# Performance work log

Measured on AMD Instinct MI355X. Metric: run time of the kernel, lower is better.

Reference implementation:

```python
import jax, jax.numpy as jnp
import numpy as np
from jax import lax

T_D = 0.7          # condensation radius
T_B = 0.2          # min beta to seed a condensate
FEATURE_LENGTH = 9 # columns of raw features before the prediction block
N_FEAT = 17        # n_ccoords = N_FEAT - 14 = 3
N_EVENTS = 16
POINTS_PER_EVENT = 65536


def setup_inputs() -> dict:
    key = jax.random.key(0)
    N = N_EVENTS * POINTS_PER_EVENT
    # uniform [0,1): betas in [0,1), ccoords in the unit cube -> realistic clustering
    x = jax.random.uniform(key, (N, N_FEAT), dtype=jnp.float32)
    row_splits = (jnp.arange(N_EVENTS + 1) * POINTS_PER_EVENT).astype(jnp.int32)
    return {"x": x, "row_splits": row_splits}


def _build_condensates(ccoords, betas, radius, min_beta):
    """Greedy NMS-like condensation, vectorized over events.
    ccoords: [E, P, C] float; betas: [E, P] float.
    Returns asso [E,P] int32 (index of assigned condensate, -1 = noise) and
    iscond [E,P] bool (condensation point flags).
    """
    E, P, _ = ccoords.shape
    r2 = radius * radius

    def masked_beta(asso):
        return jnp.where(asso < 0, betas, -1.0)

    def cond_fn(state):
        asso, _ = state
        return jnp.any(jnp.max(masked_beta(asso), axis=1) >= min_beta)

    def body_fn(state):
        asso, iscond = state
        mb = masked_beta(asso)                     # [E,P]
        ref = jnp.argmax(mb, axis=1)               # [E] highest-beta unassigned point
        valid = jnp.take_along_axis(mb, ref[:, None], axis=1)[:, 0] >= min_beta  # [E]
        refc = jnp.take_along_axis(ccoords, ref[:, None, None], axis=1)          # [E,1,C]
        distsq = jnp.sum((ccoords - refc) ** 2, axis=-1)                          # [E,P]
        assign = (asso < 0) & (distsq <= r2) & valid[:, None]
        asso = jnp.where(assign, ref[:, None].astype(jnp.int32), asso)
        newcond = (jnp.arange(P)[None, :] == ref[:, None]) & valid[:, None]
        return asso, iscond | newcond

    asso0 = jnp.full((E, P), -1, dtype=jnp.int32)
    iscond0 = jnp.zeros((E, P), dtype=jnp.bool_)
    return lax.while_loop(cond_fn, body_fn, (asso0, iscond0))


def reference(x, row_splits):
    E = row_splits.shape[0] - 1
    N, F = x.shape
    P = N // E  # uniform events (RaggedConstructTensor equivalent for equal splits)
    n_ccoords = F - 14
    x_pred = x[:, FEATURE_LENGTH:]
    n_pred = x_pred.shape[-1]
    betas = x_pred[:, 0].reshape(E, P)
    ccoords = x_pred[:, n_pred - n_ccoords:].reshape(E, P, n_ccoords)

    asso, iscond = _build_condensates(ccoords, betas, T_D, T_B)

    ncond = jnp.sum(iscond, axis=1).astype(jnp.int32)  # condensates per event
    out_row_splits = jnp.concatenate(
        [jnp.zeros((1,), jnp.int32), jnp.cumsum(ncond).astype(jnp.int32)])
    # jit-safe equivalent of dout = x[iscond > 0]: zero-mask non-condensates
    mask = iscond.reshape(-1, 1).astype(x.dtype)
    dout = x * mask  # [N, F], rows of non-condensates are zero
    return dout, out_row_splits
```

## Files before the change

### kernel.cpp

```cpp
#include <hip/hip_runtime.h>

typedef unsigned long long u64;
typedef unsigned int u32;

static constexpr int NF = 17;
static constexpr int BCOL = 9;
static constexpr int CCOL = 14;
static constexpr int CONDCAP = 256;
static constexpr int NPASS = 4;
static constexpr int RPB = 512;
static constexpr int MAXIT = 8;

#define T_B_F ((float)0.2)
#define R2_F  ((float)(0.7*0.7))

__device__ __forceinline__ u64 kmax(u64 a, u64 b){ return a > b ? a : b; }

__device__ __forceinline__ u64 shfl_down_u64(u64 v, int off){
    u32 lo = (u32)v, hi = (u32)(v >> 32);
    lo = __shfl_down(lo, off, 64);
    hi = __shfl_down(hi, off, 64);
    return ((u64)hi << 32) | lo;
}

__device__ __forceinline__ u64 waveReduceMax(u64 k){
    #pragma unroll
    for (int off = 32; off > 0; off >>= 1){
        u64 o = shfl_down_u64(k, off);
        if (o > k) k = o;
    }
    return k;
}

__device__ __forceinline__ float dist2(float cx, float cy, float cz,
                                       float rx, float ry, float rz){
    #pragma clang fp contract(off)
    float dx = cx - rx, dy = cy - ry, dz = cz - rz;
    float sx = dx * dx, sy = dy * dy, sz = dz * dz;
    return (sx + sy) + sz;
}

__device__ __forceinline__ u64 makeKey(float beta, u32 idx){
    return ((u64)__float_as_uint(beta) << 32) | (u64)(0xFFFFFFFFu - idx);
}

__global__ void k_init(u32* ws){
    int t = threadIdx.x;
    if (t < 1024) ws[t] = 0;
}

__global__ __launch_bounds__(512) void k_filter(
    const float4* __restrict__ x4, float4* __restrict__ out4,
    u64* __restrict__ argmax0, int* __restrict__ cnt0,
    float4* __restrict__ cA, int* __restrict__ iA,
    int P, int chunksPerEvent)
{
    __shared__ float lds[RPB * NF];
    __shared__ int swc[8], swb[8], sbase;
    __shared__ u64 sred[8];

    int e = blockIdx.x / chunksPerEvent;
    int chunk = blockIdx.x % chunksPerEvent;
    int rowStart = chunk * RPB;
    size_t tile4 = (size_t)blockIdx.x * (RPB * NF / 4);

    float4* lds4 = (float4*)lds;
    const int N4 = RPB * NF / 4;
    float4 z = make_float4(0.f, 0.f, 0.f, 0.f);
    for (int i = threadIdx.x; i < N4; i += 512){
        lds4[i] = x4[tile4 + i];
        out4[tile4 + i] = z;
    }
    __syncthreads();

    int tid = threadIdx.x, lid = tid & 63, wid = tid >> 6;
    float be = lds[tid*NF+BCOL];
    float cx = lds[tid*NF+CCOL], cy = lds[tid*NF+CCOL+1], cz = lds[tid*NF+CCOL+2];
    bool kp = (be >= T_B_F);
    u64 bal = __ballot(kp);
    int wcnt = __popcll(bal);
    u64 lk = kp ? makeKey(be, (u32)(rowStart + tid)) : 0;
    u64 kw = waveReduceMax(lk);
    if (lid == 0){ swc[wid] = wcnt; sred[wid] = kw; }
    __syncthreads();
    if (tid == 0){
        int tot = 0;
        for (int w = 0; w < 8; w++){ swb[w] = tot; tot += swc[w]; }
        sbase = tot ? atomicAdd(&cnt0[e], tot) : 0;
        u64 m = sred[0];
        for (int i = 1; i < 8; i++) m = kmax(m, sred[i]);
        if (m) atomicMax(&argmax0[e], m);
    }
    __syncthreads();
    if (kp){
        int pos = sbase + swb[wid] + __popcll(bal & ((1ull << lid) - 1));
        size_t eoff = (size_t)e * P;
        cA[eoff + pos] = make_float4(cx, cy, cz, be);
        iA[eoff + pos] = rowStart + tid;
    }
}

__global__ __launch_bounds__(256) void k_pass(
    const float* __restrict__ x,
    const float4* __restrict__ cIn, const int* __restrict__ iIn,
    float4* __restrict__ cOut, int* __restrict__ iOut,
    const u64* __restrict__ argmaxIn, u64* __restrict__ argmaxOut,
    const int* __restrict__ cntIn, int* __restrict__ cntOut,
    int* __restrict__ ncond, int* __restrict__ condlist,
    int P, int blocksPerEvent)
{
    __shared__ int swc[4], swb[4], sbase;
    __shared__ u64 sred[4];

    int e = blockIdx.x / blocksPerEvent;
    int c = blockIdx.x % blocksPerEvent;
    u64 key = argmaxIn[e];
    float betaRef = __uint_as_float((u32)(key >> 32));
    if (!(betaRef >= T_B_F)) return;
    u32 refIdx = 0xFFFFFFFFu - (u32)(key & 0xFFFFFFFFu);
    if (c == 0 && threadIdx.x == 0){
        int s = atomicAdd(&ncond[e], 1);
        if (s < CONDCAP) condlist[e * CONDCAP + s] = (int)refIdx;
    }
    int n = cntIn[e];
    if (c * 256 >= n) return;
    size_t rbase = ((size_t)e * P + refIdx) * NF;
    float rx = x[rbase + CCOL], ry = x[rbase + CCOL + 1], rz = x[rbase + CCOL + 2];

    int tid = threadIdx.x, lid = tid & 63, wid = tid >> 6;
    size_t eoff = (size_t)e * P;
    int stride = blocksPerEvent * 256;

    float4 cc[MAXIT]; int ix[MAXIT]; bool kp[MAXIT]; u64 bal[MAXIT];
    int wcnt = 0;
    u64 lk = 0;
    #pragma unroll
    for (int k = 0; k < MAXIT; k++){
        int i = c * 256 + tid + k * stride;
        bool inb = i < n;
        int ii = inb ? i : 0;
        cc[k] = cIn[eoff + ii];
        ix[k] = iIn[eoff + ii];
        float d2 = dist2(cc[k].x, cc[k].y, cc[k].z, rx, ry, rz);
        kp[k] = inb && !(d2 <= R2_F);
        bal[k] = __ballot(kp[k]);
        wcnt += __popcll(bal[k]);
        if (kp[k]) lk = kmax(lk, makeKey(cc[k].w, (u32)ix[k]));
    }
    u64 kw = waveReduceMax(lk);
    if (lid == 0){ swc[wid] = wcnt; sred[wid] = kw; }
    __syncthreads();
    if (tid == 0){
        int tot = 0;
        for (int w = 0; w < 4; w++){ swb[w] = tot; tot += swc[w]; }
        sbase = tot ? atomicAdd(&cntOut[e], tot) : 0;
        u64 m = sred[0];
        for (int i = 1; i < 4; i++) m = kmax(m, sred[i]);
        if (m) atomicMax(&argmaxOut[e], m);
    }
    __syncthreads();
    int pos = sbase + swb[wid];
    u64 lm = (1ull << lid) - 1;
    #pragma unroll
    for (int k = 0; k < MAXIT; k++){
        if (kp[k]){
            int p_ = pos + __popcll(bal[k] & lm);
            cOut[eoff + p_] = cc[k];
            iOut[eoff + p_] = ix[k];
        }
        pos += __popcll(bal[k]);
    }
}

__global__ __launch_bounds__(1024) void k_finish(
    const float* __restrict__ x,
    float4* cA, int* iA, float4* cB, int* iB,
    const u64* __restrict__ argmax2, const int* __restrict__ cnt2,
    int* __restrict__ ncond, int* __restrict__ condlist, int P)
{
    int e = blockIdx.x;
    __shared__ u64 sred[16];
    __shared__ int scnt;
    __shared__ u64 skey;
    __shared__ float srefc[3];

    int n = cnt2[e];
    u64 key = argmax2[e];
    float4* cIn = cA + (size_t)e * P; int* iIn = iA + (size_t)e * P;
    float4* cOut = cB + (size_t)e * P; int* iOut = iB + (size_t)e * P;
    int tid = threadIdx.x, lid = tid & 63, wid = tid >> 6;

    while (true){
        float betaRef = __uint_as_float((u32)(key >> 32));
        if (!(betaRef >= T_B_F)) break;
        u32 refIdx = 0xFFFFFFFFu - (u32)(key & 0xFFFFFFFFu);
        if (tid == 0){
            int s = atomicAdd(&ncond[e], 1);
            if (s < CONDCAP) condlist[e * CONDCAP + s] = (int)refIdx;
            size_t rbase = ((size_t)e * P + refIdx) * NF;
            srefc[0] = x[rbase + CCOL];
            srefc[1] = x[rbase + CCOL + 1];
            srefc[2] = x[rbase + CCOL + 2];
            scnt = 0;
        }
        __syncthreads();
        float rx = srefc[0], ry = srefc[1], rz = srefc[2];
        u64 localKey = 0;
        for (int i = tid; i < n; i += 1024){
            float4 cc = cIn[i]; int idx = iIn[i];
            float d2 = dist2(cc.x, cc.y, cc.z, rx, ry, rz);
            bool keep = !(d2 <= R2_F);
            u64 bal = __ballot(keep);
            int cw = __popcll(bal);
            int b_ = 0;
            if (lid == 0) b_ = cw ? atomicAdd(&scnt, cw) : 0;
            b_ = __shfl(b_, 0, 64);
            if (keep){
                int pos = b_ + __popcll(bal & ((1ull << lid) - 1));
                cOut[pos] = cc; iOut[pos] = idx;
                localKey = kmax(localKey, makeKey(cc.w, (u32)idx));
            }
        }
        u64 kw = waveReduceMax(localKey);
        if (lid == 0) sred[wid] = kw;
        __syncthreads();
        if (tid == 0){
            u64 m = 0;
            for (int i = 0; i < 16; i++) m = kmax(m, sred[i]);
            skey = m;
        }
        __syncthreads();
        key = skey;
        n = scnt;
        { float4* t = cIn; cIn = cOut; cOut = t; }
        { int* t = iIn; iIn = iOut; iOut = t; }
        __syncthreads();
    }
}

__global__ void k_out(const float* __restrict__ x, float* __restrict__ out,
                      const int* __restrict__ ncond, const int* __restrict__ condlist,
                      int P, int E)
{
    int e = blockIdx.x;
    if (e == 0 && threadIdx.x < E + 1){
        int s = 0;
        for (int i = 0; i < (int)threadIdx.x; i++) s += ncond[i];
        out[(size_t)E * P * NF + threadIdx.x] = (float)s;
    }
    int nc = ncond[e];
    if (nc > CONDCAP) nc = CONDCAP;
    int tot = nc * NF;
    for (int i = threadIdx.x; i < tot; i += blockDim.x){
        int j = i / NF, f = i - j * NF;
        int row = condlist[e * CONDCAP + j];
        size_t base = ((size_t)e * P + row) * NF;
        out[base + f] = x[base + f];
    }
}

extern "C" void kernel_launch(void* const* d_in, const int* in_sizes, int n_in,
                              void* d_out, int out_size, void* d_ws, size_t ws_size,
                              hipStream_t stream) {
    const float* x = (const float*)d_in[0];
    int N = in_sizes[0] / NF;
    int E = in_sizes[1] - 1;
    int P = N / E;
    float* out = (float*)d_out;
    char* ws = (char*)d_ws;

    u64* argmax = (u64*)ws;
    int* cnt    = (int*)(ws + 1024);
    int* ncond  = (int*)(ws + 2048);
    int* condlist = (int*)(ws + 4096);
    size_t listOff = 32768;
    size_t listElems = (size_t)E * P;
    float4* cA = (float4*)(ws + listOff);
    float4* cB = (float4*)(ws + listOff + listElems * 16);
    int* iA = (int*)(ws + listOff + listElems * 32);
    int* iB = (int*)(ws + listOff + listElems * 36);

    k_init<<<1, 1024, 0, stream>>>((u32*)ws);

    int chunksPerEvent = P / RPB;
    k_filter<<<E * chunksPerEvent, 512, 0, stream>>>(
        (const float4*)x, (float4*)out, argmax, cnt, cA, iA, P, chunksPerEvent);

    int bpe = 32;
    float4* cs[2] = {cA, cB};
    int* is[2] = {iA, iB};
    for (int r = 0; r < NPASS; r++){
        k_pass<<<E * bpe, 256, 0, stream>>>(
            x, cs[r & 1], is[r & 1], cs[(r + 1) & 1], is[(r + 1) & 1],
            argmax + r * E, argmax + (r + 1) * E,
            cnt + r * E, cnt + (r + 1) * E,
            ncond, condlist, P, bpe);
    }

    k_finish<<<E, 1024, 0, stream>>>(
        x, cA, iA, cB, iB, argmax + NPASS * E, cnt + NPASS * E, ncond, condlist, P);

    k_out<<<E, 256, 0, stream>>>(x, out, ncond, condlist, P, E);
}
```

Before: 188.2 us.

## Run greedy condensation tail in LDS, batch four refs per round, fuse output

Measured after the change: 246.4 us. 30.9% more time.

```diff
diff --git a/kernel.cpp b/kernel.cpp
--- a/kernel.cpp
+++ b/kernel.cpp
@@ -2,6 +2,7 @@
 
 typedef unsigned long long u64;
 typedef unsigned int u32;
+typedef float nfloat4 __attribute__((ext_vector_type(4)));
 
 static constexpr int NF = 17;
 static constexpr int BCOL = 9;
@@ -10,6 +11,9 @@
 static constexpr int NPASS = 4;
 static constexpr int RPB = 512;
 static constexpr int MAXIT = 8;
+static constexpr int LCAP = 7168;
+static constexpr int FT = 1024;
+static constexpr int FSLOT = 7;
 
 #define T_B_F ((float)0.2)
 #define R2_F  ((float)(0.7*0.7))
@@ -20,6 +24,13 @@
     u32 lo = (u32)v, hi = (u32)(v >> 32);
     lo = __shfl_down(lo, off, 64);
     hi = __shfl_down(hi, off, 64);
+    return ((u64)hi << 32) | lo;
+}
+
+__device__ __forceinline__ u64 shfl_u64(u64 v, int lane){
+    u32 lo = (u32)v, hi = (u32)(v >> 32);
+    lo = __shfl(lo, lane, 64);
+    hi = __shfl(hi, lane, 64);
     return ((u64)hi << 32) | lo;
 }
 
@@ -66,10 +77,10 @@
 
     float4* lds4 = (float4*)lds;
     const int N4 = RPB * NF / 4;
-    float4 z = make_float4(0.f, 0.f, 0.f, 0.f);
+    nfloat4 z = (nfloat4)0.f;
     for (int i = threadIdx.x; i < N4; i += 512){
         lds4[i] = x4[tile4 + i];
-        out4[tile4 + i] = z;
+        __builtin_nontemporal_store(z, (nfloat4*)&out4[tile4 + i]);
     }
     __syncthreads();
 
@@ -175,28 +186,39 @@
 __global__ __launch_bounds__(1024) void k_finish(
     const float* __restrict__ x,
     float4* cA, int* iA, float4* cB, int* iB,
-    const u64* __restrict__ argmax2, const int* __restrict__ cnt2,
-    int* __restrict__ ncond, int* __restrict__ condlist, int P)
+    const u64* __restrict__ argmaxN, const int* __restrict__ cntN,
+    int* __restrict__ ncond, const int* __restrict__ condlistG,
+    int* __restrict__ done, float* __restrict__ out, int P, int E)
 {
+    __shared__ u64 skey[LCAP];
+    __shared__ float sx[LCAP], sy[LCAP], sz[LCAP];
+    __shared__ u64 sred[16];
+    __shared__ u64 wtopk[16*4];
+    __shared__ int wtopp[16*4];
+    __shared__ int condL[CONDCAP];
+    __shared__ float refs[4][3];
+    __shared__ int scnt, snc, snacc;
+    __shared__ u64 skeyb;
+    __shared__ float srefc[3];
+
     int e = blockIdx.x;
-    __shared__ u64 sred[16];
-    __shared__ int scnt;
-    __shared__ u64 skey;
-    __shared__ float srefc[3];
-
-    int n = cnt2[e];
-    u64 key = argmax2[e];
+    int tid = threadIdx.x, lid = tid & 63, wid = tid >> 6;
+    int n = cntN[e];
+    u64 key = argmaxN[e];
     float4* cIn = cA + (size_t)e * P; int* iIn = iA + (size_t)e * P;
     float4* cOut = cB + (size_t)e * P; int* iOut = iB + (size_t)e * P;
-    int tid = threadIdx.x, lid = tid & 63, wid = tid >> 6;
-
-    while (true){
+
+    if (tid == 0) snc = ncond[e];
+    for (int i = tid; i < CONDCAP; i += FT) condL[i] = condlistG[e * CONDCAP + i];
+    __syncthreads();
+
+    while (n > LCAP){
         float betaRef = __uint_as_float((u32)(key >> 32));
         if (!(betaRef >= T_B_F)) break;
         u32 refIdx = 0xFFFFFFFFu - (u32)(key & 0xFFFFFFFFu);
         if (tid == 0){
-            int s = atomicAdd(&ncond[e], 1);
-            if (s < CONDCAP) condlist[e * CONDCAP + s] = (int)refIdx;
+            if (snc < CONDCAP) condL[snc] = (int)refIdx;
+            snc++;
             size_t rbase = ((size_t)e * P + refIdx) * NF;
             srefc[0] = x[rbase + CCOL];
             srefc[1] = x[rbase + CCOL + 1];
@@ -206,7 +228,7 @@
         __syncthreads();
         float rx = srefc[0], ry = srefc[1], rz = srefc[2];
         u64 localKey = 0;
-        for (int i = tid; i < n; i += 1024){
+        for (int i = tid; i < n; i += FT){
             float4 cc = cIn[i]; int idx = iIn[i];
             float d2 = dist2(cc.x, cc.y, cc.z, rx, ry, rz);
             bool keep = !(d2 <= R2_F);
@@ -227,35 +249,139 @@
         if (tid == 0){
             u64 m = 0;
             for (int i = 0; i < 16; i++) m = kmax(m, sred[i]);
-            skey = m;
+            skeyb = m;
         }
         __syncthreads();
-        key = skey;
-        n = scnt;
+        key = skeyb; n = scnt;
         { float4* t = cIn; cIn = cOut; cOut = t; }
         { int* t = iIn; iIn = iOut; iOut = t; }
         __syncthreads();
     }
-}
-
-__global__ void k_out(const float* __restrict__ x, float* __restrict__ out,
-                      const int* __restrict__ ncond, const int* __restrict__ condlist,
-                      int P, int E)
-{
-    int e = blockIdx.x;
-    if (e == 0 && threadIdx.x < E + 1){
-        int s = 0;
-        for (int i = 0; i < (int)threadIdx.x; i++) s += ncond[i];
-        out[(size_t)E * P * NF + threadIdx.x] = (float)s;
-    }
-    int nc = ncond[e];
-    if (nc > CONDCAP) nc = CONDCAP;
-    int tot = nc * NF;
-    for (int i = threadIdx.x; i < tot; i += blockDim.x){
+
+    float betaRef0 = __uint_as_float((u32)(key >> 32));
+    if (betaRef0 >= T_B_F && n > 0){
+        for (int i = tid; i < n; i += FT){
+            float4 cc = cIn[i]; int idx = iIn[i];
+            skey[i] = makeKey(cc.w, (u32)idx);
+            sx[i] = cc.x; sy[i] = cc.y; sz[i] = cc.z;
+        }
+        __syncthreads();
+
+        while (n > 0){
+            u64 myk[FSLOT]; int myp[FSLOT]; int mc = 0;
+            for (int i = tid; i < n; i += FT){ myk[mc] = skey[i]; myp[mc] = i; mc++; }
+            u64 excl = ~0ull;
+            #pragma unroll
+            for (int j = 0; j < 4; j++){
+                u64 lk = 0; int lp = 0;
+                #pragma unroll
+                for (int k = 0; k < FSLOT; k++)
+                    if (k < mc && myk[k] < excl && myk[k] > lk){ lk = myk[k]; lp = myp[k]; }
+                #pragma unroll
+                for (int off = 32; off > 0; off >>= 1){
+                    u64 ok = shfl_down_u64(lk, off);
+                    int op = __shfl_down(lp, off, 64);
+                    if (ok > lk){ lk = ok; lp = op; }
+                }
+                if (lid == 0){ wtopk[wid*4 + j] = lk; wtopp[wid*4 + j] = lp; }
+                excl = shfl_u64(lk, 0);
+            }
+            __syncthreads();
+
+            if (tid == 0){
+                int na = 0;
+                u64 ex = ~0ull;
+                for (int rsel = 0; rsel < 4; rsel++){
+                    u64 m = 0; int mp = 0;
+                    for (int t = 0; t < 64; t++){
+                        u64 kk2 = wtopk[t];
+                        if (kk2 < ex && kk2 > m){ m = kk2; mp = wtopp[t]; }
+                    }
+                    if (m == 0) break;
+                    ex = m;
+                    float cx2 = sx[mp], cy2 = sy[mp], cz2 = sz[mp];
+                    bool ok = true;
+                    #pragma unroll
+                    for (int a = 0; a < 4; a++)
+                        if (a < na && dist2(cx2, cy2, cz2,
+                                            refs[a][0], refs[a][1], refs[a][2]) <= R2_F)
+                            ok = false;
+                    if (ok){
+                        u32 idx2 = 0xFFFFFFFFu - (u32)(m & 0xFFFFFFFFu);
+                        if (snc < CONDCAP) condL[snc] = (int)idx2;
+                        snc++;
+                        refs[na][0] = cx2; refs[na][1] = cy2; refs[na][2] = cz2;
+                        na++;
+                    }
+                }
+                snacc = na; scnt = 0;
+            }
+            __syncthreads();
+
+            int na = snacc;
+            float rx_[4], ry_[4], rz_[4];
+            #pragma unroll
+            for (int a = 0; a < 4; a++){ rx_[a] = refs[a][0]; ry_[a] = refs[a][1]; rz_[a] = refs[a][2]; }
+            u64 kk[FSLOT]; float xx[FSLOT], yy[FSLOT], zz[FSLOT];
+            bool kp[FSLOT]; u64 bal[FSLOT];
+            int wcnt = 0;
+            #pragma unroll
+            for (int k = 0; k < FSLOT; k++){
+                int i = tid + k * FT;
+                bool inb = i < n;
+                int ii = inb ? i : 0;
+                kk[k] = skey[ii]; xx[k] = sx[ii]; yy[k] = sy[ii]; zz[k] = sz[ii];
+                bool keep = inb;
+                #pragma unroll
+                for (int a = 0; a < 4; a++)
+                    if (a < na && dist2(xx[k], yy[k], zz[k], rx_[a], ry_[a], rz_[a]) <= R2_F)
+                        keep = false;
+                kp[k] = keep;
+                bal[k] = __ballot(keep);
+                wcnt += __popcll(bal[k]);
+            }
+            int wb = 0;
+            if (lid == 0) wb = wcnt ? atomicAdd(&scnt, wcnt) : 0;
+            wb = __shfl(wb, 0, 64);
+            __syncthreads();
+
+            int posr = wb;
+            u64 lm = (1ull << lid) - 1;
+            #pragma unroll
+            for (int k = 0; k < FSLOT; k++){
+                if (kp[k]){
+                    int p_ = posr + __popcll(bal[k] & lm);
+                    skey[p_] = kk[k]; sx[p_] = xx[k]; sy[p_] = yy[k]; sz[p_] = zz[k];
+                }
+                posr += __popcll(bal[k]);
+            }
+            __syncthreads();
+            n = scnt;
+        }
+    }
+    __syncthreads();
+
+    int ncT = snc;
+    int ncc = ncT > CONDCAP ? CONDCAP : ncT;
+    for (int i = tid; i < ncc * NF; i += FT){
         int j = i / NF, f = i - j * NF;
-        int row = condlist[e * CONDCAP + j];
+        int row = condL[j];
         size_t base = ((size_t)e * P + row) * NF;
         out[base + f] = x[base + f];
+    }
+    if (tid == 0){
+        ncond[e] = ncT;
+        __threadfence();
+        int r = atomicAdd(done, 1);
+        if (r == E - 1){
+            size_t ob = (size_t)E * P * NF;
+            int s = 0;
+            out[ob] = 0.0f;
+            for (int i = 0; i < E; i++){
+                s += atomicAdd(&ncond[i], 0);
+                out[ob + i + 1] = (float)s;
+            }
+        }
     }
 }
 
@@ -272,6 +398,7 @@
     u64* argmax = (u64*)ws;
     int* cnt    = (int*)(ws + 1024);
     int* ncond  = (int*)(ws + 2048);
+    int* done   = (int*)(ws + 2560);
     int* condlist = (int*)(ws + 4096);
     size_t listOff = 32768;
     size_t listElems = (size_t)E * P;
@@ -298,7 +425,6 @@
     }
 
     k_finish<<<E, 1024, 0, stream>>>(
-        x, cA, iA, cB, iB, argmax + NPASS * E, cnt + NPASS * E, ncond, condlist, P);
-
-    k_out<<<E, 256, 0, stream>>>(x, out, ncond, condlist, P, E);
-}
+        x, cA, iA, cB, iB, argmax + NPASS * E, cnt + NPASS * E,
+        ncond, condlist, done, out, P, E);
+}
```

## Fuse condensation passes into one per-event kernel with LDS single-wave tail

Applied to the files above, without the earlier changes.

New measurement: 228.0 us. +21.1%, slower.

```diff
diff --git a/kernel.cpp b/kernel.cpp
--- a/kernel.cpp
+++ b/kernel.cpp
@@ -6,10 +6,10 @@
 static constexpr int NF = 17;
 static constexpr int BCOL = 9;
 static constexpr int CCOL = 14;
-static constexpr int CONDCAP = 256;
-static constexpr int NPASS = 4;
+static constexpr int CONDCAP = 1024;
 static constexpr int RPB = 512;
-static constexpr int MAXIT = 8;
+static constexpr int LCAP = 7168;
+static constexpr int FT = 1024;
 
 #define T_B_F ((float)0.2)
 #define R2_F  ((float)(0.7*0.7))
@@ -20,6 +20,13 @@
     u32 lo = (u32)v, hi = (u32)(v >> 32);
     lo = __shfl_down(lo, off, 64);
     hi = __shfl_down(hi, off, 64);
+    return ((u64)hi << 32) | lo;
+}
+
+__device__ __forceinline__ u64 shfl_u64(u64 v, int lane){
+    u32 lo = (u32)v, hi = (u32)(v >> 32);
+    lo = __shfl(lo, lane, 64);
+    hi = __shfl(hi, lane, 64);
     return ((u64)hi << 32) | lo;
 }
 
@@ -100,103 +107,38 @@
     }
 }
 
-__global__ __launch_bounds__(256) void k_pass(
-    const float* __restrict__ x,
-    const float4* __restrict__ cIn, const int* __restrict__ iIn,
-    float4* __restrict__ cOut, int* __restrict__ iOut,
-    const u64* __restrict__ argmaxIn, u64* __restrict__ argmaxOut,
-    const int* __restrict__ cntIn, int* __restrict__ cntOut,
-    int* __restrict__ ncond, int* __restrict__ condlist,
-    int P, int blocksPerEvent)
-{
-    __shared__ int swc[4], swb[4], sbase;
-    __shared__ u64 sred[4];
-
-    int e = blockIdx.x / blocksPerEvent;
-    int c = blockIdx.x % blocksPerEvent;
-    u64 key = argmaxIn[e];
-    float betaRef = __uint_as_float((u32)(key >> 32));
-    if (!(betaRef >= T_B_F)) return;
-    u32 refIdx = 0xFFFFFFFFu - (u32)(key & 0xFFFFFFFFu);
-    if (c == 0 && threadIdx.x == 0){
-        int s = atomicAdd(&ncond[e], 1);
-        if (s < CONDCAP) condlist[e * CONDCAP + s] = (int)refIdx;
-    }
-    int n = cntIn[e];
-    if (c * 256 >= n) return;
-    size_t rbase = ((size_t)e * P + refIdx) * NF;
-    float rx = x[rbase + CCOL], ry = x[rbase + CCOL + 1], rz = x[rbase + CCOL + 2];
-
-    int tid = threadIdx.x, lid = tid & 63, wid = tid >> 6;
-    size_t eoff = (size_t)e * P;
-    int stride = blocksPerEvent * 256;
-
-    float4 cc[MAXIT]; int ix[MAXIT]; bool kp[MAXIT]; u64 bal[MAXIT];
-    int wcnt = 0;
-    u64 lk = 0;
-    #pragma unroll
-    for (int k = 0; k < MAXIT; k++){
-        int i = c * 256 + tid + k * stride;
-        bool inb = i < n;
-        int ii = inb ? i : 0;
-        cc[k] = cIn[eoff + ii];
-        ix[k] = iIn[eoff + ii];
-        float d2 = dist2(cc[k].x, cc[k].y, cc[k].z, rx, ry, rz);
-        kp[k] = inb && !(d2 <= R2_F);
-        bal[k] = __ballot(kp[k]);
-        wcnt += __popcll(bal[k]);
-        if (kp[k]) lk = kmax(lk, makeKey(cc[k].w, (u32)ix[k]));
-    }
-    u64 kw = waveReduceMax(lk);
-    if (lid == 0){ swc[wid] = wcnt; sred[wid] = kw; }
-    __syncthreads();
-    if (tid == 0){
-        int tot = 0;
-        for (int w = 0; w < 4; w++){ swb[w] = tot; tot += swc[w]; }
-        sbase = tot ? atomicAdd(&cntOut[e], tot) : 0;
-        u64 m = sred[0];
-        for (int i = 1; i < 4; i++) m = kmax(m, sred[i]);
-        if (m) atomicMax(&argmaxOut[e], m);
-    }
-    __syncthreads();
-    int pos = sbase + swb[wid];
-    u64 lm = (1ull << lid) - 1;
-    #pragma unroll
-    for (int k = 0; k < MAXIT; k++){
-        if (kp[k]){
-            int p_ = pos + __popcll(bal[k] & lm);
-            cOut[eoff + p_] = cc[k];
-            iOut[eoff + p_] = ix[k];
-        }
-        pos += __popcll(bal[k]);
-    }
-}
-
 __global__ __launch_bounds__(1024) void k_finish(
     const float* __restrict__ x,
     float4* cA, int* iA, float4* cB, int* iB,
-    const u64* __restrict__ argmax2, const int* __restrict__ cnt2,
-    int* __restrict__ ncond, int* __restrict__ condlist, int P)
+    const u64* __restrict__ argmax0, const int* __restrict__ cnt0,
+    int* __restrict__ ncond, int* __restrict__ done,
+    float* __restrict__ out, int P, int E)
 {
+    __shared__ u64 skey[LCAP];
+    __shared__ float sx[LCAP], sy[LCAP], sz[LCAP];
+    __shared__ u64 sred[16];
+    __shared__ int condL[CONDCAP];
+    __shared__ int scnt, snc;
+    __shared__ u64 skeyb;
+    __shared__ float srefc[3];
+
     int e = blockIdx.x;
-    __shared__ u64 sred[16];
-    __shared__ int scnt;
-    __shared__ u64 skey;
-    __shared__ float srefc[3];
-
-    int n = cnt2[e];
-    u64 key = argmax2[e];
+    int tid = threadIdx.x, lid = tid & 63, wid = tid >> 6;
+    int n = cnt0[e];
+    u64 key = argmax0[e];
     float4* cIn = cA + (size_t)e * P; int* iIn = iA + (size_t)e * P;
     float4* cOut = cB + (size_t)e * P; int* iOut = iB + (size_t)e * P;
-    int tid = threadIdx.x, lid = tid & 63, wid = tid >> 6;
-
-    while (true){
+
+    if (tid == 0) snc = 0;
+    __syncthreads();
+
+    while (n > LCAP){
         float betaRef = __uint_as_float((u32)(key >> 32));
         if (!(betaRef >= T_B_F)) break;
         u32 refIdx = 0xFFFFFFFFu - (u32)(key & 0xFFFFFFFFu);
         if (tid == 0){
-            int s = atomicAdd(&ncond[e], 1);
-            if (s < CONDCAP) condlist[e * CONDCAP + s] = (int)refIdx;
+            if (snc < CONDCAP) condL[snc] = (int)refIdx;
+            snc++;
             size_t rbase = ((size_t)e * P + refIdx) * NF;
             srefc[0] = x[rbase + CCOL];
             srefc[1] = x[rbase + CCOL + 1];
@@ -206,7 +148,7 @@
         __syncthreads();
         float rx = srefc[0], ry = srefc[1], rz = srefc[2];
         u64 localKey = 0;
-        for (int i = tid; i < n; i += 1024){
+        for (int i = tid; i < n; i += FT){
             float4 cc = cIn[i]; int idx = iIn[i];
             float d2 = dist2(cc.x, cc.y, cc.z, rx, ry, rz);
             bool keep = !(d2 <= R2_F);
@@ -227,35 +169,93 @@
         if (tid == 0){
             u64 m = 0;
             for (int i = 0; i < 16; i++) m = kmax(m, sred[i]);
-            skey = m;
-        }
-        __syncthreads();
-        key = skey;
-        n = scnt;
+            skeyb = m;
+        }
+        __syncthreads();
+        key = skeyb; n = scnt;
         { float4* t = cIn; cIn = cOut; cOut = t; }
         { int* t = iIn; iIn = iOut; iOut = t; }
         __syncthreads();
     }
-}
-
-__global__ void k_out(const float* __restrict__ x, float* __restrict__ out,
-                      const int* __restrict__ ncond, const int* __restrict__ condlist,
-                      int P, int E)
-{
-    int e = blockIdx.x;
-    if (e == 0 && threadIdx.x < E + 1){
-        int s = 0;
-        for (int i = 0; i < (int)threadIdx.x; i++) s += ncond[i];
-        out[(size_t)E * P * NF + threadIdx.x] = (float)s;
-    }
-    int nc = ncond[e];
-    if (nc > CONDCAP) nc = CONDCAP;
-    int tot = nc * NF;
-    for (int i = threadIdx.x; i < tot; i += blockDim.x){
+
+    float betaRef0 = __uint_as_float((u32)(key >> 32));
+    if (betaRef0 >= T_B_F && n > 0){
+        for (int i = tid; i < n; i += FT){
+            float4 cc = cIn[i]; int idx = iIn[i];
+            skey[i] = makeKey(cc.w, (u32)idx);
+            sx[i] = cc.x; sy[i] = cc.y; sz[i] = cc.z;
+        }
+        __syncthreads();
+
+        if (wid == 0){
+            int snc_l = snc;
+            int mp = -1;
+            while (true){
+                float betaRef = __uint_as_float((u32)(key >> 32));
+                if (!(betaRef >= T_B_F)) break;
+                u32 refIdx = 0xFFFFFFFFu - (u32)(key & 0xFFFFFFFFu);
+                if (lid == 0 && snc_l < CONDCAP) condL[snc_l] = (int)refIdx;
+                snc_l++;
+                float rx, ry, rz;
+                if (mp >= 0){ rx = sx[mp]; ry = sy[mp]; rz = sz[mp]; }
+                else {
+                    size_t rbase = ((size_t)e * P + refIdx) * NF;
+                    rx = x[rbase + CCOL]; ry = x[rbase + CCOL + 1]; rz = x[rbase + CCOL + 2];
+                }
+                u64 bk = 0; int bp = -1;
+                int alive = 0;
+                for (int i0 = 0; i0 < n; i0 += 64){
+                    int i = i0 + lid;
+                    bool inb = i < n;
+                    int ii = inb ? i : 0;
+                    u64 k = skey[ii];
+                    float xx = sx[ii], yy = sy[ii], zz = sz[ii];
+                    float d2 = dist2(xx, yy, zz, rx, ry, rz);
+                    bool keep = inb && !(d2 <= R2_F);
+                    u64 b = __ballot(keep);
+                    if (keep){
+                        int pos = alive + __popcll(b & ((1ull << lid) - 1));
+                        skey[pos] = k; sx[pos] = xx; sy[pos] = yy; sz[pos] = zz;
+                        if (k > bk){ bk = k; bp = pos; }
+                    }
+                    alive += __popcll(b);
+                }
+                #pragma unroll
+                for (int off = 32; off > 0; off >>= 1){
+                    u64 ok = shfl_down_u64(bk, off);
+                    int op = __shfl_down(bp, off, 64);
+                    if (ok > bk){ bk = ok; bp = op; }
+                }
+                key = shfl_u64(bk, 0);
+                mp = __shfl(bp, 0, 64);
+                n = alive;
+            }
+            if (lid == 0) snc = snc_l;
+        }
+    }
+    __syncthreads();
+
+    int ncT = snc;
+    int ncc = ncT > CONDCAP ? CONDCAP : ncT;
+    for (int i = tid; i < ncc * NF; i += FT){
         int j = i / NF, f = i - j * NF;
-        int row = condlist[e * CONDCAP + j];
+        int row = condL[j];
         size_t base = ((size_t)e * P + row) * NF;
         out[base + f] = x[base + f];
+    }
+    if (tid == 0){
+        ncond[e] = ncT;
+        __threadfence();
+        int r = atomicAdd(done, 1);
+        if (r == E - 1){
+            size_t ob = (size_t)E * P * NF;
+            int s = 0;
+            out[ob] = 0.0f;
+            for (int i = 0; i < E; i++){
+                s += atomicAdd(&ncond[i], 0);
+                out[ob + i + 1] = (float)s;
+            }
+        }
     }
 }
 
@@ -272,7 +272,7 @@
     u64* argmax = (u64*)ws;
     int* cnt    = (int*)(ws + 1024);
     int* ncond  = (int*)(ws + 2048);
-    int* condlist = (int*)(ws + 4096);
+    int* done   = (int*)(ws + 2560);
     size_t listOff = 32768;
     size_t listElems = (size_t)E * P;
     float4* cA = (float4*)(ws + listOff);
@@ -286,19 +286,6 @@
     k_filter<<<E * chunksPerEvent, 512, 0, stream>>>(
         (const float4*)x, (float4*)out, argmax, cnt, cA, iA, P, chunksPerEvent);
 
-    int bpe = 32;
-    float4* cs[2] = {cA, cB};
-    int* is[2] = {iA, iB};
-    for (int r = 0; r < NPASS; r++){
-        k_pass<<<E * bpe, 256, 0, stream>>>(
-            x, cs[r & 1], is[r & 1], cs[(r + 1) & 1], is[(r + 1) & 1],
-            argmax + r * E, argmax + (r + 1) * E,
-            cnt + r * E, cnt + (r + 1) * E,
-            ncond, condlist, P, bpe);
-    }
-
     k_finish<<<E, 1024, 0, stream>>>(
-        x, cA, iA, cB, iB, argmax + NPASS * E, cnt + NPASS * E, ncond, condlist, P);
-
-    k_out<<<E, 256, 0, stream>>>(x, out, ncond, condlist, P, E);
-}
+        x, cA, iA, cB, iB, argmax, cnt, ncond, done, out, P, E);
+}
```
